# Kernel tuning notes

Hardware: AMD Instinct MI355X
Metric: run time of the kernel (lower is better)

## Reference

```python
import jax, jax.numpy as jnp
import numpy as np
from jax import lax

NB, HH, WW, C = 8, 64, 64, 192
G, K, DW_K, PA_K = 12, 3, 5, 3
GC, P = C // G, K * K
PAD, STRIDE, DIL = 1, 1, 1
OFFSET_SCALE = 1.0
LN_EPS = 1e-5


def _grid_sample(img, grid):
    # img: (B,Cc,H,W); grid: (B,L,P,2) xy in [-1,1]; bilinear, zeros padding, align_corners=False
    B, Cc, H, W = img.shape
    gx = (grid[..., 0] + 1.0) * (W * 0.5) - 0.5
    gy = (grid[..., 1] + 1.0) * (H * 0.5) - 0.5
    x0, y0 = jnp.floor(gx), jnp.floor(gy)

    def gather(xi, yi):
        valid = (xi >= 0) & (xi <= W - 1) & (yi >= 0) & (yi <= H - 1)
        xc = jnp.clip(xi, 0, W - 1).astype(jnp.int32)
        yc = jnp.clip(yi, 0, H - 1).astype(jnp.int32)
        v = jax.vmap(lambda im, y, x: im[:, y, x])(img, yc, xc)  # (B,Cc,L,P)
        return v * valid[:, None].astype(img.dtype)

    wx1, wy1 = gx - x0, gy - y0
    wx0, wy0 = 1.0 - wx1, 1.0 - wy1
    return (gather(x0, y0) * (wx0 * wy0)[:, None]
            + gather(x0 + 1.0, y0) * (wx1 * wy0)[:, None]
            + gather(x0, y0 + 1.0) * (wx0 * wy1)[:, None]
            + gather(x0 + 1.0, y0 + 1.0) * (wx1 * wy1)[:, None])


def _dcnv3_core(x, offset, mask):
    # x: (N,H,W,C) projected input; offset: (N,H,W,G*P*2); mask: (N,H,W,G*P)
    N, H, W, _ = x.shape
    xp = jnp.pad(x, ((0, 0), (PAD, PAD), (PAD, PAD), (0, 0)))
    Hp, Wp = H + 2 * PAD, W + 2 * PAD
    Ho, Wo = offset.shape[1], offset.shape[2]
    base = (DIL * (K - 1)) // 2 + 0.5
    ref_y = (base + jnp.arange(Ho) * STRIDE) / Hp
    ref_x = (base + jnp.arange(Wo) * STRIDE) / Wp
    ref = jnp.stack(jnp.broadcast_arrays(ref_x[None, :], ref_y[:, None]), -1)  # (Ho,Wo,2) xy
    start = -((DIL * (K - 1)) // 2)
    pts = (start + jnp.arange(K) * DIL).astype(x.dtype)
    gxg = jnp.broadcast_to((pts / Wp)[:, None], (K, K))  # w offset varies along dim0 (torch order)
    gyg = jnp.broadcast_to((pts / Hp)[None, :], (K, K))
    grid = jnp.tile(jnp.stack([gxg, gyg], -1).reshape(P, 2), (G, 1))  # (G*P,2)
    loc = ref[None, :, :, None, :] + grid * OFFSET_SCALE  # (1,Ho,Wo,G*P,2)
    norm = jnp.array([Wp, Hp], dtype=x.dtype)
    loc = loc + offset.reshape(N, Ho, Wo, G * P, 2) * OFFSET_SCALE / norm
    sg = 2.0 * loc - 1.0  # (N,Ho,Wo,G*P,2)
    img = xp.reshape(N, Hp * Wp, G, GC).transpose(0, 2, 3, 1).reshape(N * G, GC, Hp, Wp)
    grd = sg.reshape(N, Ho * Wo, G, P, 2).transpose(0, 2, 1, 3, 4).reshape(N * G, Ho * Wo, P, 2)
    samp = _grid_sample(img, grd)  # (N*G, GC, L, P)
    m = mask.reshape(N, Ho * Wo, G, P).transpose(0, 2, 1, 3).reshape(N * G, 1, Ho * Wo, P)
    out = (samp * m).sum(-1)  # (N*G, GC, L)
    return out.reshape(N, G, GC, Ho * Wo).transpose(0, 3, 1, 2).reshape(N, Ho, Wo, C)


def _dcnv3(x, dw_w, dw_b, ln_g, ln_b, off_w, off_b, msk_w, msk_b, in_w, in_b, out_w, out_b, cfs_w, cfs_b):
    N, H, W, _ = x.shape
    x_proj = x @ in_w + in_b
    # depthwise conv (5x5) -> LayerNorm (channels_last) -> GELU(exact)
    u = lax.conv_general_dilated(x, dw_w, (1, 1), 'SAME',
                                 dimension_numbers=('NHWC', 'HWIO', 'NHWC'),
                                 feature_group_count=C) + dw_b
    mu = u.mean(-1, keepdims=True)
    var = ((u - mu) ** 2).mean(-1, keepdims=True)
    u = (u - mu) * lax.rsqrt(var + LN_EPS) * ln_g + ln_b
    u = jax.nn.gelu(u, approximate=False)
    offset = u @ off_w + off_b  # (N,H,W,G*P*2)
    m = jax.nn.softmax((u @ msk_w + msk_b).reshape(N, H, W, G, P), axis=-1).reshape(N, H, W, G * P)
    y = _dcnv3_core(x_proj, offset, m)
    cfs = jax.nn.sigmoid(u @ cfs_w + cfs_b)  # (N,H,W,G)
    cfs = jnp.repeat(cfs, GC, axis=-1)       # (N,H,W,C), group-blockwise
    y = y * (1.0 - cfs) + x_proj * cfs
    return y @ out_w + out_b


def _patch_attention(x):
    # x: (N,H,W,C) -> std over softmax'd 3x3 neighbor scores: (N,H,W)
    N, H, W, _ = x.shape
    pad = (PA_K - 1) // 2
    xp = jnp.pad(x, ((0, 0), (pad, pad), (pad, pad), (0, 0)))
    neigh = jnp.stack([xp[:, i:i + H, j:j + W, :] for i in range(PA_K) for j in range(PA_K)],
                      axis=-1)  # (N,H,W,C,K1*K2), torch unfold ordering
    scores = jnp.einsum('nhwc,nhwck->nhwk', x, neigh)
    sm = jax.nn.softmax(scores, axis=-1)
    return jnp.std(sm, axis=-1, ddof=1)  # torch.std is unbiased


def setup_inputs() -> dict:
    key = jax.random.key(0)
    ks = jax.random.split(key, 8)
    s = 0.02
    return {
        'x': jax.random.normal(ks[0], (NB, HH, WW, C), jnp.float32),
        'dw_w': jax.random.normal(ks[1], (DW_K, DW_K, 1, C), jnp.float32) * s,
        'dw_b': jnp.zeros((C,), jnp.float32),
        'ln_g': jnp.ones((C,), jnp.float32),
        'ln_b': jnp.zeros((C,), jnp.float32),
        'off_w': jax.random.normal(ks[2], (C, G * P * 2), jnp.float32) * s,
        'off_b': jnp.zeros((G * P * 2,), jnp.float32),
        'msk_w': jax.random.normal(ks[3], (C, G * P), jnp.float32) * s,
        'msk_b': jnp.zeros((G * P,), jnp.float32),
        'in_w': jax.random.normal(ks[4], (C, C), jnp.float32) * s,
        'in_b': jnp.zeros((C,), jnp.float32),
        'out_w': jax.random.normal(ks[5], (C, C), jnp.float32) * s,
        'out_b': jnp.zeros((C,), jnp.float32),
        'cfs_w': jax.random.normal(ks[6], (C, G), jnp.float32) * s,
        'cfs_b': jnp.zeros((G,), jnp.float32),
    }


def reference(x, dw_w, dw_b, ln_g, ln_b, off_w, off_b, msk_w, msk_b, in_w, in_b, out_w, out_b, cfs_w, cfs_b):
    x1 = _dcnv3(x, dw_w, dw_b, ln_g, ln_b, off_w, off_b, msk_w, msk_b, in_w, in_b, out_w, out_b, cfs_w, cfs_b)
    mask = _patch_attention(x1)           # (N,H,W)
    return x + x1 * mask[..., None]
```

## Files before the change

kernel.cpp:

```cpp
#include <hip/hip_runtime.h>
#include <hip/hip_bf16.h>
#include <math.h>

#define NB 8
#define HH 64
#define WW 64
#define C 192
#define G 12
#define GC 16
#define P 9
#define NPIX (NB*HH*WW)

typedef __attribute__((ext_vector_type(8))) short short8;
typedef __attribute__((ext_vector_type(4))) float f32x4;
typedef unsigned short ushort;

__device__ __forceinline__ ushort to_bf16(float f) {
  __hip_bfloat16 b = __float2bfloat16(f);
  return *(ushort*)&b;
}
__device__ __forceinline__ float bf2f(ushort u) {
  union { unsigned u; float f; } cv; cv.u = ((unsigned)u) << 16; return cv.f;
}
__device__ __forceinline__ float bflo(unsigned u) {
  union { unsigned v; float f; } c; c.v = u << 16; return c.f;
}
__device__ __forceinline__ float bfhi(unsigned u) {
  union { unsigned v; float f; } c; c.v = u & 0xffff0000u; return c.f;
}

__global__ void prep_w_kernel(const float* __restrict__ in_w, const float* __restrict__ out_w,
    const float* __restrict__ off_w, const float* __restrict__ msk_w, const float* __restrict__ cfs_w,
    const float* __restrict__ off_b, const float* __restrict__ msk_b, const float* __restrict__ cfs_b,
    ushort* __restrict__ in_wt, ushort* __restrict__ out_wt, ushort* __restrict__ wf_t,
    float* __restrict__ bf_bias) {
  int idx = blockIdx.x*256 + threadIdx.x;
  if (idx < 36864) {
    int n = idx/192, k = idx%192;
    in_wt[idx] = to_bf16(in_w[k*192 + n]);
  } else if (idx < 73728) {
    int j = idx - 36864; int n = j/192, k = j%192;
    out_wt[j] = to_bf16(out_w[k*192 + n]);
  } else if (idx < 147456) {
    int j = idx - 73728; int n = j/192, k = j%192;
    float v = 0.f;
    if (n < 216)      v = off_w[k*216 + n];
    else if (n < 324) v = msk_w[k*108 + (n-216)];
    else if (n < 336) v = cfs_w[k*12  + (n-324)];
    wf_t[j] = to_bf16(v);
  }
  if (idx < 384) {
    float b = 0.f;
    if (idx < 216)      b = off_b[idx];
    else if (idx < 324) b = msk_b[idx-216];
    else if (idx < 336) b = cfs_b[idx-324];
    bf_bias[idx] = b;
  }
}

template<int NW, int NSTORE, bool BF16OUT, bool AF32>
__global__ __launch_bounds__(256) void mfma_gemm(const void* __restrict__ A_,
    const ushort* __restrict__ Wt, const float* __restrict__ bias,
    void* __restrict__ Cout_) {
  __shared__ ushort As[4*64*8];
  __shared__ ushort Bs[4*64*8];
  int pix0 = blockIdx.x * 64, n0 = blockIdx.y * 64;
  int tid = threadIdx.x;
  int wid = tid >> 6, lane = tid & 63;
  int wr = wid >> 1, wc = wid & 1;
  int lr = lane >> 4, lc = lane & 15;

  f32x4 acc[2][2];
  #pragma unroll
  for (int m=0;m<2;m++)
    #pragma unroll
    for (int j=0;j<2;j++) acc[m][j] = (f32x4){0.f,0.f,0.f,0.f};

  int s_kb = tid >> 6, s_row = tid & 63;

  short8 pa, pb;
  auto load_tile = [&](int k0) {
    if (AF32) {
      const float* Af = (const float*)A_;
      float4 u0 = *(const float4*)&Af[(size_t)(pix0 + s_row)*192 + k0 + s_kb*8];
      float4 u1 = *(const float4*)&Af[(size_t)(pix0 + s_row)*192 + k0 + s_kb*8 + 4];
      pa[0]=to_bf16(u0.x); pa[1]=to_bf16(u0.y); pa[2]=to_bf16(u0.z); pa[3]=to_bf16(u0.w);
      pa[4]=to_bf16(u1.x); pa[5]=to_bf16(u1.y); pa[6]=to_bf16(u1.z); pa[7]=to_bf16(u1.w);
    } else {
      const ushort* Ab = (const ushort*)A_;
      pa = *(const short8*)&Ab[(size_t)(pix0 + s_row)*192 + k0 + s_kb*8];
    }
    pb = *(const short8*)&Wt[(size_t)(n0 + s_row)*192 + k0 + s_kb*8];
  };
  load_tile(0);

  for (int t = 0; t < 6; t++) {
    __syncthreads();
    *(short8*)&As[(size_t)tid*8] = pa;
    *(short8*)&Bs[(size_t)tid*8] = pb;
    __syncthreads();
    if (t < 5) load_tile((t+1)*32);
    short8 a0 = *(const short8*)&As[(size_t)(lr*64 + wr*32 + lc)*8];
    short8 a1 = *(const short8*)&As[(size_t)(lr*64 + wr*32 + 16 + lc)*8];
    short8 b0 = *(const short8*)&Bs[(size_t)(lr*64 + wc*32 + lc)*8];
    short8 b1 = *(const short8*)&Bs[(size_t)(lr*64 + wc*32 + 16 + lc)*8];
    acc[0][0] = __builtin_amdgcn_mfma_f32_16x16x32_bf16(a0, b0, acc[0][0], 0,0,0);
    acc[0][1] = __builtin_amdgcn_mfma_f32_16x16x32_bf16(a0, b1, acc[0][1], 0,0,0);
    acc[1][0] = __builtin_amdgcn_mfma_f32_16x16x32_bf16(a1, b0, acc[1][0], 0,0,0);
    acc[1][1] = __builtin_amdgcn_mfma_f32_16x16x32_bf16(a1, b1, acc[1][1], 0,0,0);
  }
  #pragma unroll
  for (int j=0;j<2;j++) {
    int col = n0 + wc*32 + j*16 + lc;
    if (NW != NSTORE && col >= NSTORE) continue;
    float bb = bias[col];
    #pragma unroll
    for (int m=0;m<2;m++) {
      size_t rbase = pix0 + wr*32 + m*16 + lr*4;
      #pragma unroll
      for (int r=0;r<4;r++) {
        float v = acc[m][j][r] + bb;
        if (BF16OUT) ((ushort*)Cout_)[(rbase + r)*NSTORE + col] = to_bf16(v);
        else         ((float*) Cout_)[(rbase + r)*NSTORE + col] = v;
      }
    }
  }
}

#define SEG 16
__global__ __launch_bounds__(192) void dw_ln_gelu_kernel(const float* __restrict__ x,
    const float* __restrict__ dw_w, const float* __restrict__ dw_b,
    const float* __restrict__ ln_g, const float* __restrict__ ln_b,
    ushort* __restrict__ u_out) {
  int blk = blockIdx.x;
  int qw = blk & 3; int nh = blk >> 2;
  int h = nh & 63, n = nh >> 6;
  int c = threadIdx.x;
  int w0 = qw * SEG;

  float kw[25];
  #pragma unroll
  for (int t=0;t<25;t++) kw[t] = dw_w[t*C + c];

  float acc[SEG];
  float bb = dw_b[c];
  #pragma unroll
  for (int i=0;i<SEG;i++) acc[i] = bb;

  #pragma unroll
  for (int i=0;i<5;i++) {
    int hy = h + i - 2;
    if (hy < 0 || hy >= HH) continue;
    const float* rowp = &x[(((size_t)n*HH + hy)*WW)*C + c];
    #pragma unroll
    for (int wi=0; wi<SEG+4; wi++) {
      int w_in = w0 - 2 + wi;
      if (w_in < 0 || w_in >= WW) continue;
      float v = rowp[(size_t)w_in*C];
      #pragma unroll
      for (int j=0;j<5;j++) {
        int a = wi - j;
        if (a >= 0 && a < SEG) acc[a] += v * kw[i*5+j];
      }
    }
  }

  __shared__ float lds_acc[SEG][C+1];
  __shared__ float part1[SEG][12], part2[SEG][12];
  __shared__ float mu_s[SEG], rs_s[SEG];
  #pragma unroll
  for (int i=0;i<SEG;i++) lds_acc[i][c] = acc[i];
  __syncthreads();
  {
    int p = threadIdx.x & 15, chunk = threadIdx.x >> 4;
    float s1 = 0.f, s2 = 0.f;
    #pragma unroll
    for (int k=0;k<16;k++) {
      float v = lds_acc[p][chunk*16 + k];
      s1 += v; s2 += v*v;
    }
    part1[p][chunk] = s1; part2[p][chunk] = s2;
  }
  __syncthreads();
  if (threadIdx.x < SEG) {
    int p = threadIdx.x;
    float t1 = 0.f, t2 = 0.f;
    #pragma unroll
    for (int k=0;k<12;k++){ t1 += part1[p][k]; t2 += part2[p][k]; }
    float mu = t1 * (1.0f/C);
    float var = t2 * (1.0f/C) - mu*mu;
    mu_s[p] = mu; rs_s[p] = rsqrtf(var + 1e-5f);
  }
  __syncthreads();
  float gg = ln_g[c], lb = ln_b[c];
  size_t obase = ((size_t)nh*WW + w0)*C + c;
  #pragma unroll
  for (int i=0;i<SEG;i++) {
    float uv = (acc[i] - mu_s[i])*rs_s[i]*gg + lb;
    uv = 0.5f*uv*(1.0f + erff(uv*0.70710678118654752f));
    u_out[obase + (size_t)i*C] = to_bf16(uv);
  }
}

#define SPX 8
__device__ __forceinline__ void fma8(float* acc, float w, uint4 q) {
  acc[0] += w*bflo(q.x); acc[1] += w*bfhi(q.x);
  acc[2] += w*bflo(q.y); acc[3] += w*bfhi(q.y);
  acc[4] += w*bflo(q.z); acc[5] += w*bfhi(q.z);
  acc[6] += w*bflo(q.w); acc[7] += w*bfhi(q.w);
}
__global__ __launch_bounds__(192) void sample_kernel(const ushort* __restrict__ omc,
    const ushort* __restrict__ x_proj, ushort* __restrict__ y_out) {
  int pix0 = blockIdx.x * SPX;
  int n = pix0 >> 12;
  int hw = pix0 & 4095; int h = hw >> 6; int w0 = hw & 63;
  int tid = threadIdx.x;
  __shared__ int   addrs[SPX*108*4];
  __shared__ float wts[SPX*108*4];
  __shared__ float msm[SPX][108];
  __shared__ float cfss[SPX][12];

  for (int i = tid; i < SPX*108; i += 192) {
    int px = i / 108, gp = i % 108;
    int p = gp % 9;
    const float pts[3] = {-1.f, 0.f, 1.f};
    unsigned off2 = ((const unsigned*)omc)[(size_t)(pix0+px)*168 + gp];
    float ox = bflo(off2), oy = bfhi(off2);
    float gx = 1.0f + (float)(w0+px) + pts[p/3] + ox;
    float gy = 1.0f + (float)h + pts[p%3] + oy;
    float x0f = floorf(gx), y0f = floorf(gy);
    float wx1 = gx - x0f, wy1 = gy - y0f;
    float wx0 = 1.f-wx1, wy0 = 1.f-wy1;
    int x0 = (int)x0f, y0 = (int)y0f;
    bool xv0 = (x0   >= 1) && (x0   <= 64);
    bool xv1 = (x0+1 >= 1) && (x0+1 <= 64);
    bool yv0 = (y0   >= 1) && (y0   <= 64);
    bool yv1 = (y0+1 >= 1) && (y0+1 <= 64);
    int base = n*HH*WW*C;
    int4 a4;
    a4.x = (yv0&&xv0) ? (base + ((y0-1)*WW + (x0-1))*C)*2 : 0;
    a4.y = (yv0&&xv1) ? (base + ((y0-1)*WW + (x0  ))*C)*2 : 0;
    a4.z = (yv1&&xv0) ? (base + ((y0  )*WW + (x0-1))*C)*2 : 0;
    a4.w = (yv1&&xv1) ? (base + ((y0  )*WW + (x0  ))*C)*2 : 0;
    ((int4*)addrs)[i] = a4;
    float4 w4;
    w4.x = (yv0&&xv0) ? wx0*wy0 : 0.f;
    w4.y = (yv0&&xv1) ? wx1*wy0 : 0.f;
    w4.z = (yv1&&xv0) ? wx0*wy1 : 0.f;
    w4.w = (yv1&&xv1) ? wx1*wy1 : 0.f;
    ((float4*)wts)[i] = w4;
  }
  if (tid < SPX*12) {
    int px = tid / 12, gg = tid % 12;
    const ushort* mrow = &omc[(size_t)(pix0+px)*336 + 216 + gg*9];
    float lv[P];
    #pragma unroll
    for (int p=0;p<P;p++) lv[p] = bf2f(mrow[p]);
    float m = -1e30f;
    #pragma unroll
    for (int p=0;p<P;p++) m = fmaxf(m, lv[p]);
    float e[P]; float s = 0.f;
    #pragma unroll
    for (int p=0;p<P;p++){ e[p] = expf(lv[p]-m); s += e[p]; }
    float inv = 1.0f/s;
    #pragma unroll
    for (int p=0;p<P;p++) msm[px][gg*9+p] = e[p]*inv;
  } else {
    int q = tid - SPX*12;
    int px = q / 12, gg = q % 12;
    cfss[px][gg] = 1.0f/(1.0f+expf(-bf2f(omc[(size_t)(pix0+px)*336 + 324 + gg])));
  }
  __syncthreads();
  for (int i = tid; i < SPX*108; i += 192) {
    int px = i / 108, gp = i % 108;
    float m = msm[px][gp] * (1.0f - cfss[px][gp/9]);
    f32x4 w4 = *(f32x4*)&wts[i*4];
    w4 *= m;
    *(f32x4*)&wts[i*4] = w4;
  }
  __syncthreads();
  int px = tid / 24, s = tid - (tid/24)*24;
  int g = s >> 1;
  int cb = s * 16;
  const char* xb = (const char*)x_proj;
  float acc[8] = {0.f,0.f,0.f,0.f,0.f,0.f,0.f,0.f};
  #pragma unroll
  for (int pb = 0; pb < 3; pb++) {
    int gp = g*9 + pb*3;
    int4 a0 = ((const int4*)addrs)[px*108+gp];
    int4 a1 = ((const int4*)addrs)[px*108+gp+1];
    int4 a2 = ((const int4*)addrs)[px*108+gp+2];
    float4 wv0 = ((const float4*)wts)[px*108+gp];
    float4 wv1 = ((const float4*)wts)[px*108+gp+1];
    float4 wv2 = ((const float4*)wts)[px*108+gp+2];
    uint4 t00 = *(const uint4*)(xb + (unsigned)(a0.x + cb));
    uint4 t01 = *(const uint4*)(xb + (unsigned)(a0.y + cb));
    uint4 t02 = *(const uint4*)(xb + (unsigned)(a0.z + cb));
    uint4 t03 = *(const uint4*)(xb + (unsigned)(a0.w + cb));
    uint4 t10 = *(const uint4*)(xb + (unsigned)(a1.x + cb));
    uint4 t11 = *(const uint4*)(xb + (unsigned)(a1.y + cb));
    uint4 t12 = *(const uint4*)(xb + (unsigned)(a1.z + cb));
    uint4 t13 = *(const uint4*)(xb + (unsigned)(a1.w + cb));
    uint4 t20 = *(const uint4*)(xb + (unsigned)(a2.x + cb));
    uint4 t21 = *(const uint4*)(xb + (unsigned)(a2.y + cb));
    uint4 t22 = *(const uint4*)(xb + (unsigned)(a2.z + cb));
    uint4 t23 = *(const uint4*)(xb + (unsigned)(a2.w + cb));
    fma8(acc, wv0.x, t00); fma8(acc, wv0.y, t01);
    fma8(acc, wv0.z, t02); fma8(acc, wv0.w, t03);
    fma8(acc, wv1.x, t10); fma8(acc, wv1.y, t11);
    fma8(acc, wv1.z, t12); fma8(acc, wv1.w, t13);
    fma8(acc, wv2.x, t20); fma8(acc, wv2.y, t21);
    fma8(acc, wv2.z, t22); fma8(acc, wv2.w, t23);
  }
  float cf = cfss[px][g];
  uint4 qx = *(const uint4*)(xb + ((size_t)(pix0+px)*C)*2 + cb);
  fma8(acc, cf, qx);
  short8 r;
  #pragma unroll
  for (int k=0;k<8;k++) r[k] = to_bf16(acc[k]);
  *(short8*)&y_out[(size_t)(pix0+px)*C + s*8] = r;
}

__global__ __launch_bounds__(256) void pattn_kernel(const float* __restrict__ x,
    const ushort* __restrict__ x1, float* __restrict__ out) {
  __shared__ unsigned xs[100*97];
  __shared__ float psc[64][36];
  __shared__ float sd_s[64];
  int blk = blockIdx.x;
  int n = blk >> 6;
  int ty = (blk >> 3) & 7, tx = blk & 7;
  int th0 = ty*8, tw0 = tx*8;
  int tid = threadIdx.x;
  const unsigned* x1u = (const unsigned*)x1;
  for (int i = tid; i < 100*96; i += 256) {
    int cell = i / 96, wd = i - cell*96;
    int gy = th0 - 1 + cell/10, gx = tw0 - 1 + cell%10;
    unsigned v = 0;
    if (gy>=0 && gy<HH && gx>=0 && gx<WW)
      v = x1u[(((size_t)n*HH+gy)*WW+gx)*96 + wd];
    xs[cell*97 + wd] = v;
  }
  __syncthreads();
  {
    int px = tid >> 2, qq = tid & 3;
    int py = px >> 3, pxx = px & 7;
    int cell = (py+1)*10 + (pxx+1);
    float cen[48];
    #pragma unroll
    for (int k=0;k<24;k++) {
      unsigned w = xs[cell*97 + qq*24 + k];
      cen[2*k] = bflo(w); cen[2*k+1] = bfhi(w);
    }
    #pragma unroll
    for (int ni=0;ni<9;ni++) {
      int nc = cell + (ni/3-1)*10 + (ni%3-1);
      float a = 0.f;
      #pragma unroll
      for (int k=0;k<24;k++) {
        unsigned w = xs[nc*97 + qq*24 + k];
        a += cen[2*k]*bflo(w) + cen[2*k+1]*bfhi(w);
      }
      psc[px][qq*9+ni] = a;
    }
  }
  __syncthreads();
  if (tid < 64) {
    float sc[9];
    #pragma unroll
    for (int k=0;k<9;k++)
      sc[k] = psc[tid][k] + psc[tid][9+k] + psc[tid][18+k] + psc[tid][27+k];
    float m = sc[0];
    #pragma unroll
    for (int k=1;k<9;k++) m = fmaxf(m, sc[k]);
    float pr[9]; float s = 0.f;
    #pragma unroll
    for (int k=0;k<9;k++){ pr[k] = expf(sc[k]-m); s += pr[k]; }
    float inv = 1.0f/s;
    float mean = 0.f;
    #pragma unroll
    for (int k=0;k<9;k++){ pr[k] *= inv; mean += pr[k]; }
    mean *= (1.0f/9.0f);
    float var = 0.f;
    #pragma unroll
    for (int k=0;k<9;k++){ float d = pr[k]-mean; var += d*d; }
    sd_s[tid] = sqrtf(var*(1.0f/8.0f));
  }
  __syncthreads();
  for (int i = tid; i < 64*96; i += 256) {
    int p2 = i / 96, wd = i - p2*96;
    int py2 = p2 >> 3, px2 = p2 & 7;
    unsigned v = xs[((py2+1)*10 + (px2+1))*97 + wd];
    size_t pix = ((size_t)n*HH + th0+py2)*WW + tw0+px2;
    float2 xv = ((const float2*)x)[pix*96 + wd];
    float sd = sd_s[p2];
    float2 o; o.x = xv.x + bflo(v)*sd; o.y = xv.y + bfhi(v)*sd;
    ((float2*)out)[pix*96 + wd] = o;
  }
}

extern "C" void kernel_launch(void* const* d_in, const int* in_sizes, int n_in,
                              void* d_out, int out_size, void* d_ws, size_t ws_size,
                              hipStream_t stream) {
  const float* x     = (const float*)d_in[0];
  const float* dw_w  = (const float*)d_in[1];
  const float* dw_b  = (const float*)d_in[2];
  const float* ln_g  = (const float*)d_in[3];
  const float* ln_b  = (const float*)d_in[4];
  const float* off_w = (const float*)d_in[5];
  const float* off_b = (const float*)d_in[6];
  const float* msk_w = (const float*)d_in[7];
  const float* msk_b = (const float*)d_in[8];
  const float* in_w  = (const float*)d_in[9];
  const float* in_b  = (const float*)d_in[10];
  const float* out_w = (const float*)d_in[11];
  const float* out_b = (const float*)d_in[12];
  const float* cfs_w = (const float*)d_in[13];
  const float* cfs_b = (const float*)d_in[14];
  float* outp = (float*)d_out;

  ushort* omc    = (ushort*)d_ws;
  ushort* xproj  = omc + (size_t)NPIX*336;
  ushort* x1_bf  = xproj + (size_t)NPIX*192;
  ushort* u_bf   = x1_bf + (size_t)NPIX*192;
  ushort* in_wt  = u_bf + (size_t)NPIX*192;
  ushort* out_wt = in_wt + 192*192;
  ushort* wf_t   = out_wt + 192*192;
  float*  bfb    = (float*)(wf_t + 384*192);

  prep_w_kernel<<<(147456+255)/256, 256, 0, stream>>>(in_w, out_w, off_w, msk_w, cfs_w,
                                                       off_b, msk_b, cfs_b,
                                                       in_wt, out_wt, wf_t, bfb);
  mfma_gemm<192,192,true,true><<<dim3(NPIX/64, 3), 256, 0, stream>>>(x, in_wt, in_b, xproj);
  dw_ln_gelu_kernel<<<NB*HH*4, 192, 0, stream>>>(x, dw_w, dw_b, ln_g, ln_b, u_bf);
  mfma_gemm<384,336,true,false><<<dim3(NPIX/64, 6), 256, 0, stream>>>(u_bf, wf_t, bfb, omc);
  sample_kernel<<<NPIX/SPX, 192, 0, stream>>>(omc, xproj, u_bf);
  mfma_gemm<192,192,true,false><<<dim3(NPIX/64, 3), 256, 0, stream>>>(u_bf, out_wt, out_b, x1_bf);
  pattn_kernel<<<NB*64, 256, 0, stream>>>(x, x1_bf, outp);
}
```

Measured before the change: 159.4 us.

## Merge input GEMM with depthwise LN-GELU launch and compact sampling weights

Combines the input-projection GEMM and the depthwise conv + LayerNorm + GELU kernel into one launch, with blocks split by index and dw blocks padded to 256 threads. This lets the two independent stages run concurrently and removes a launch boundary. The sampling kernel now stores bilinear weights as bf16 in shared memory and folds softmax and the (1-cf) scale directly into them, dropping the msm buffer and one pass. It also swizzles the block-to-pixel mapping. The bf16 weights lower precision, and the merged kernel leaves 64 idle threads in each dw block while sharing register and LDS budgets across both bodies.

```diff
diff --git a/kernel.cpp b/kernel.cpp
--- a/kernel.cpp
+++ b/kernel.cpp
@@ -59,12 +59,12 @@
 }
 
 template<int NW, int NSTORE, bool BF16OUT, bool AF32>
-__global__ __launch_bounds__(256) void mfma_gemm(const void* __restrict__ A_,
+__device__ __forceinline__ void gemm_body(const void* __restrict__ A_,
     const ushort* __restrict__ Wt, const float* __restrict__ bias,
-    void* __restrict__ Cout_) {
+    void* __restrict__ Cout_, int bx, int by) {
   __shared__ ushort As[4*64*8];
   __shared__ ushort Bs[4*64*8];
-  int pix0 = blockIdx.x * 64, n0 = blockIdx.y * 64;
+  int pix0 = bx * 64, n0 = by * 64;
   int tid = threadIdx.x;
   int wid = tid >> 6, lane = tid & 63;
   int wr = wid >> 1, wc = wid & 1;
@@ -127,40 +127,47 @@
   }
 }
 
+template<int NW, int NSTORE, bool BF16OUT, bool AF32>
+__global__ __launch_bounds__(256) void mfma_gemm(const void* __restrict__ A_,
+    const ushort* __restrict__ Wt, const float* __restrict__ bias,
+    void* __restrict__ Cout_) {
+  gemm_body<NW,NSTORE,BF16OUT,AF32>(A_, Wt, bias, Cout_, blockIdx.x, blockIdx.y);
+}
+
 #define SEG 16
-__global__ __launch_bounds__(192) void dw_ln_gelu_kernel(const float* __restrict__ x,
+__device__ __forceinline__ void dwln_body(const float* __restrict__ x,
     const float* __restrict__ dw_w, const float* __restrict__ dw_b,
     const float* __restrict__ ln_g, const float* __restrict__ ln_b,
-    ushort* __restrict__ u_out) {
-  int blk = blockIdx.x;
+    ushort* __restrict__ u_out, int blk) {
   int qw = blk & 3; int nh = blk >> 2;
   int h = nh & 63, n = nh >> 6;
   int c = threadIdx.x;
   int w0 = qw * SEG;
+  bool act = (c < 192);
 
   float kw[25];
-  #pragma unroll
-  for (int t=0;t<25;t++) kw[t] = dw_w[t*C + c];
-
   float acc[SEG];
-  float bb = dw_b[c];
-  #pragma unroll
-  for (int i=0;i<SEG;i++) acc[i] = bb;
-
-  #pragma unroll
-  for (int i=0;i<5;i++) {
-    int hy = h + i - 2;
-    if (hy < 0 || hy >= HH) continue;
-    const float* rowp = &x[(((size_t)n*HH + hy)*WW)*C + c];
-    #pragma unroll
-    for (int wi=0; wi<SEG+4; wi++) {
-      int w_in = w0 - 2 + wi;
-      if (w_in < 0 || w_in >= WW) continue;
-      float v = rowp[(size_t)w_in*C];
+  if (act) {
+    #pragma unroll
+    for (int t=0;t<25;t++) kw[t] = dw_w[t*C + c];
+    float bb = dw_b[c];
+    #pragma unroll
+    for (int i=0;i<SEG;i++) acc[i] = bb;
+    #pragma unroll
+    for (int i=0;i<5;i++) {
+      int hy = h + i - 2;
+      if (hy < 0 || hy >= HH) continue;
+      const float* rowp = &x[(((size_t)n*HH + hy)*WW)*C + c];
       #pragma unroll
-      for (int j=0;j<5;j++) {
-        int a = wi - j;
-        if (a >= 0 && a < SEG) acc[a] += v * kw[i*5+j];
+      for (int wi=0; wi<SEG+4; wi++) {
+        int w_in = w0 - 2 + wi;
+        if (w_in < 0 || w_in >= WW) continue;
+        float v = rowp[(size_t)w_in*C];
+        #pragma unroll
+        for (int j=0;j<5;j++) {
+          int a = wi - j;
+          if (a >= 0 && a < SEG) acc[a] += v * kw[i*5+j];
+        }
       }
     }
   }
@@ -168,11 +175,13 @@
   __shared__ float lds_acc[SEG][C+1];
   __shared__ float part1[SEG][12], part2[SEG][12];
   __shared__ float mu_s[SEG], rs_s[SEG];
-  #pragma unroll
-  for (int i=0;i<SEG;i++) lds_acc[i][c] = acc[i];
-  __syncthreads();
-  {
-    int p = threadIdx.x & 15, chunk = threadIdx.x >> 4;
+  if (act) {
+    #pragma unroll
+    for (int i=0;i<SEG;i++) lds_acc[i][c] = acc[i];
+  }
+  __syncthreads();
+  if (c < 192) {
+    int p = c & 15, chunk = c >> 4;
     float s1 = 0.f, s2 = 0.f;
     #pragma unroll
     for (int k=0;k<16;k++) {
@@ -182,23 +191,38 @@
     part1[p][chunk] = s1; part2[p][chunk] = s2;
   }
   __syncthreads();
-  if (threadIdx.x < SEG) {
-    int p = threadIdx.x;
+  if (c < SEG) {
     float t1 = 0.f, t2 = 0.f;
     #pragma unroll
-    for (int k=0;k<12;k++){ t1 += part1[p][k]; t2 += part2[p][k]; }
+    for (int k=0;k<12;k++){ t1 += part1[c][k]; t2 += part2[c][k]; }
     float mu = t1 * (1.0f/C);
     float var = t2 * (1.0f/C) - mu*mu;
-    mu_s[p] = mu; rs_s[p] = rsqrtf(var + 1e-5f);
-  }
-  __syncthreads();
-  float gg = ln_g[c], lb = ln_b[c];
-  size_t obase = ((size_t)nh*WW + w0)*C + c;
-  #pragma unroll
-  for (int i=0;i<SEG;i++) {
-    float uv = (acc[i] - mu_s[i])*rs_s[i]*gg + lb;
-    uv = 0.5f*uv*(1.0f + erff(uv*0.70710678118654752f));
-    u_out[obase + (size_t)i*C] = to_bf16(uv);
+    mu_s[c] = mu; rs_s[c] = rsqrtf(var + 1e-5f);
+  }
+  __syncthreads();
+  if (act) {
+    float gg = ln_g[c], lb = ln_b[c];
+    size_t obase = ((size_t)nh*WW + w0)*C + c;
+    #pragma unroll
+    for (int i=0;i<SEG;i++) {
+      float uv = (acc[i] - mu_s[i])*rs_s[i]*gg + lb;
+      uv = 0.5f*uv*(1.0f + erff(uv*0.70710678118654752f));
+      u_out[obase + (size_t)i*C] = to_bf16(uv);
+    }
+  }
+}
+
+__global__ __launch_bounds__(256) void fat1_kernel(const float* __restrict__ x,
+    const ushort* __restrict__ in_wt, const float* __restrict__ in_b,
+    ushort* __restrict__ xproj,
+    const float* __restrict__ dw_w, const float* __restrict__ dw_b,
+    const float* __restrict__ ln_g, const float* __restrict__ ln_b,
+    ushort* __restrict__ u_out) {
+  int b = blockIdx.x;
+  if (b < 1536) {
+    gemm_body<192,192,true,true>(x, in_wt, in_b, xproj, b & 511, b >> 9);
+  } else {
+    dwln_body(x, dw_w, dw_b, ln_g, ln_b, u_out, b - 1536);
   }
 }
 
@@ -211,14 +235,15 @@
 }
 __global__ __launch_bounds__(192) void sample_kernel(const ushort* __restrict__ omc,
     const ushort* __restrict__ x_proj, ushort* __restrict__ y_out) {
-  int pix0 = blockIdx.x * SPX;
+  int bid = blockIdx.x;
+  int swz = (bid & 7) * 512 + (bid >> 3);
+  int pix0 = swz * SPX;
   int n = pix0 >> 12;
   int hw = pix0 & 4095; int h = hw >> 6; int w0 = hw & 63;
   int tid = threadIdx.x;
-  __shared__ int   addrs[SPX*108*4];
-  __shared__ float wts[SPX*108*4];
-  __shared__ float msm[SPX][108];
-  __shared__ float cfss[SPX][12];
+  __shared__ int    addrs[SPX*108*4];
+  __shared__ ushort wts16[SPX*108*4];
+  __shared__ float  cfss[SPX][12];
 
   for (int i = tid; i < SPX*108; i += 192) {
     int px = i / 108, gp = i % 108;
@@ -243,13 +268,14 @@
     a4.z = (yv1&&xv0) ? (base + ((y0  )*WW + (x0-1))*C)*2 : 0;
     a4.w = (yv1&&xv1) ? (base + ((y0  )*WW + (x0  ))*C)*2 : 0;
     ((int4*)addrs)[i] = a4;
-    float4 w4;
-    w4.x = (yv0&&xv0) ? wx0*wy0 : 0.f;
-    w4.y = (yv0&&xv1) ? wx1*wy0 : 0.f;
-    w4.z = (yv1&&xv0) ? wx0*wy1 : 0.f;
-    w4.w = (yv1&&xv1) ? wx1*wy1 : 0.f;
-    ((float4*)wts)[i] = w4;
-  }
+    ushort4 w4;
+    w4.x = to_bf16((yv0&&xv0) ? wx0*wy0 : 0.f);
+    w4.y = to_bf16((yv0&&xv1) ? wx1*wy0 : 0.f);
+    w4.z = to_bf16((yv1&&xv0) ? wx0*wy1 : 0.f);
+    w4.w = to_bf16((yv1&&xv1) ? wx1*wy1 : 0.f);
+    ((ushort4*)wts16)[i] = w4;
+  }
+  __syncthreads();
   if (tid < SPX*12) {
     int px = tid / 12, gg = tid % 12;
     const ushort* mrow = &omc[(size_t)(pix0+px)*336 + 216 + gg*9];
@@ -259,24 +285,23 @@
     float m = -1e30f;
     #pragma unroll
     for (int p=0;p<P;p++) m = fmaxf(m, lv[p]);
-    float e[P]; float s = 0.f;
-    #pragma unroll
-    for (int p=0;p<P;p++){ e[p] = expf(lv[p]-m); s += e[p]; }
-    float inv = 1.0f/s;
-    #pragma unroll
-    for (int p=0;p<P;p++) msm[px][gg*9+p] = e[p]*inv;
-  } else {
-    int q = tid - SPX*12;
-    int px = q / 12, gg = q % 12;
-    cfss[px][gg] = 1.0f/(1.0f+expf(-bf2f(omc[(size_t)(pix0+px)*336 + 324 + gg])));
-  }
-  __syncthreads();
-  for (int i = tid; i < SPX*108; i += 192) {
-    int px = i / 108, gp = i % 108;
-    float m = msm[px][gp] * (1.0f - cfss[px][gp/9]);
-    f32x4 w4 = *(f32x4*)&wts[i*4];
-    w4 *= m;
-    *(f32x4*)&wts[i*4] = w4;
+    float s = 0.f;
+    #pragma unroll
+    for (int p=0;p<P;p++){ lv[p] = expf(lv[p]-m); s += lv[p]; }
+    float cf = 1.0f/(1.0f+expf(-bf2f(omc[(size_t)(pix0+px)*336 + 324 + gg])));
+    cfss[px][gg] = cf;
+    float onem = (1.0f - cf) / s;
+    #pragma unroll
+    for (int p=0;p<P;p++) {
+      int i = px*108 + gg*9 + p;
+      float mp = lv[p]*onem;
+      ushort4 w4 = ((const ushort4*)wts16)[i];
+      w4.x = to_bf16(bf2f(w4.x)*mp);
+      w4.y = to_bf16(bf2f(w4.y)*mp);
+      w4.z = to_bf16(bf2f(w4.z)*mp);
+      w4.w = to_bf16(bf2f(w4.w)*mp);
+      ((ushort4*)wts16)[i] = w4;
+    }
   }
   __syncthreads();
   int px = tid / 24, s = tid - (tid/24)*24;
@@ -290,9 +315,9 @@
     int4 a0 = ((const int4*)addrs)[px*108+gp];
     int4 a1 = ((const int4*)addrs)[px*108+gp+1];
     int4 a2 = ((const int4*)addrs)[px*108+gp+2];
-    float4 wv0 = ((const float4*)wts)[px*108+gp];
-    float4 wv1 = ((const float4*)wts)[px*108+gp+1];
-    float4 wv2 = ((const float4*)wts)[px*108+gp+2];
+    ushort4 u0 = ((const ushort4*)wts16)[px*108+gp];
+    ushort4 u1 = ((const ushort4*)wts16)[px*108+gp+1];
+    ushort4 u2 = ((const ushort4*)wts16)[px*108+gp+2];
     uint4 t00 = *(const uint4*)(xb + (unsigned)(a0.x + cb));
     uint4 t01 = *(const uint4*)(xb + (unsigned)(a0.y + cb));
     uint4 t02 = *(const uint4*)(xb + (unsigned)(a0.z + cb));
@@ -305,12 +330,12 @@
     uint4 t21 = *(const uint4*)(xb + (unsigned)(a2.y + cb));
     uint4 t22 = *(const uint4*)(xb + (unsigned)(a2.z + cb));
     uint4 t23 = *(const uint4*)(xb + (unsigned)(a2.w + cb));
-    fma8(acc, wv0.x, t00); fma8(acc, wv0.y, t01);
-    fma8(acc, wv0.z, t02); fma8(acc, wv0.w, t03);
-    fma8(acc, wv1.x, t10); fma8(acc, wv1.y, t11);
-    fma8(acc, wv1.z, t12); fma8(acc, wv1.w, t13);
-    fma8(acc, wv2.x, t20); fma8(acc, wv2.y, t21);
-    fma8(acc, wv2.z, t22); fma8(acc, wv2.w, t23);
+    fma8(acc, bf2f(u0.x), t00); fma8(acc, bf2f(u0.y), t01);
+    fma8(acc, bf2f(u0.z), t02); fma8(acc, bf2f(u0.w), t03);
+    fma8(acc, bf2f(u1.x), t10); fma8(acc, bf2f(u1.y), t11);
+    fma8(acc, bf2f(u1.z), t12); fma8(acc, bf2f(u1.w), t13);
+    fma8(acc, bf2f(u2.x), t20); fma8(acc, bf2f(u2.y), t21);
+    fma8(acc, bf2f(u2.z), t22); fma8(acc, bf2f(u2.w), t23);
   }
   float cf = cfss[px][g];
   uint4 qx = *(const uint4*)(xb + ((size_t)(pix0+px)*C)*2 + cb);
@@ -430,8 +455,8 @@
   prep_w_kernel<<<(147456+255)/256, 256, 0, stream>>>(in_w, out_w, off_w, msk_w, cfs_w,
                                                        off_b, msk_b, cfs_b,
                                                        in_wt, out_wt, wf_t, bfb);
-  mfma_gemm<192,192,true,true><<<dim3(NPIX/64, 3), 256, 0, stream>>>(x, in_wt, in_b, xproj);
-  dw_ln_gelu_kernel<<<NB*HH*4, 192, 0, stream>>>(x, dw_w, dw_b, ln_g, ln_b, u_bf);
+  fat1_kernel<<<1536 + NB*HH*4, 256, 0, stream>>>(x, in_wt, in_b, xproj,
+                                                   dw_w, dw_b, ln_g, ln_b, u_bf);
   mfma_gemm<384,336,true,false><<<dim3(NPIX/64, 6), 256, 0, stream>>>(u_bf, wf_t, bfb, omc);
   sample_kernel<<<NPIX/SPX, 192, 0, stream>>>(omc, xproj, u_bf);
   mfma_gemm<192,192,true,false><<<dim3(NPIX/64, 3), 256, 0, stream>>>(u_bf, out_wt, out_b, x1_bf);
```

New measurement: 154.5 us. 1.03x faster.
